# Kernel tuning notes

Measured on AMD Instinct MI355X. Metric: run time of the kernel, lower is better.

## Reference

```python
import jax, jax.numpy as jnp
import numpy as np

B, N, E = 2, 30000, 120000
IN_F, OUT_F, H = 512, 512, 4
D = OUT_F // H  # head_dim = 128
LN_EPS = 1e-5


def setup_inputs() -> dict:
    key = jax.random.key(0)
    k1, k2, k3, k4 = jax.random.split(key, 4)
    node_features = jax.random.normal(k1, (B, N, IN_F), dtype=jnp.float32)
    edge_index = jax.random.randint(k2, (2, E), 0, N, dtype=jnp.int64)
    # per-head linear transforms (bias=False): W[h] is [in_features, head_dim]
    W = jax.random.normal(k3, (H, IN_F, D), dtype=jnp.float32) / np.sqrt(IN_F)
    # per-head attention vectors a[h] is [2*head_dim] (Linear(2*head_dim,1,bias=False))
    a = jax.random.normal(k4, (H, 2 * D), dtype=jnp.float32) / np.sqrt(2 * D)
    ln_gamma = jnp.ones((OUT_F,), dtype=jnp.float32)
    ln_beta = jnp.zeros((OUT_F,), dtype=jnp.float32)
    return {"node_features": node_features, "edge_index": edge_index,
            "W": W, "a": a, "ln_gamma": ln_gamma, "ln_beta": ln_beta}


def reference(node_features, edge_index, W, a, ln_gamma, ln_beta):
    src, dst = edge_index[0], edge_index[1]
    # all-heads linear transform: [B, H, N, D]
    t = jnp.einsum('bni,hid->bhnd', node_features, W)
    # per-edge gathered features: [B, H, E, D]
    sf = t[:, :, src, :]
    df = t[:, :, dst, :]
    # attention score = [sf ; df] . a  == sf.a_src + df.a_dst  -> [B, H, E]
    scores = (jnp.einsum('bhed,hd->bhe', sf, a[:, :D])
              + jnp.einsum('bhed,hd->bhe', df, a[:, D:]))
    scores = jax.nn.leaky_relu(scores, negative_slope=0.2)
    # NOTE: faithful to source — softmax over ALL edges (dim=-1), not per-dst
    w = jax.nn.softmax(scores, axis=-1)
    # scatter-add aggregation into destination nodes (the Python-loop in torch)
    agg = jnp.zeros_like(t).at[:, :, dst, :].add(w[..., None] * sf)  # [B,H,N,D]
    # concat heads along feature dim (head order preserved)
    out = jnp.transpose(agg, (0, 2, 1, 3)).reshape(node_features.shape[0], N, H * D)
    # LayerNorm over last dim
    mu = jnp.mean(out, axis=-1, keepdims=True)
    var = jnp.mean(jnp.square(out - mu), axis=-1, keepdims=True)
    out = (out - mu) * jax.lax.rsqrt(var + LN_EPS) * ln_gamma + ln_beta
    return out
```

## Files before the change

### kernel.cpp

```cpp
#include <hip/hip_runtime.h>
#include <stdint.h>

#define Bn 2
#define Nn 30000
#define En 120000
#define KIN 512
#define Hh 4
#define Dd 128
#define MROWS 60000
#define MPAD  60032
#define LNEPS 1e-5f
#define EBLK 469

typedef unsigned short u16;
typedef unsigned int   u32;
typedef __attribute__((ext_vector_type(8))) short short8;
typedef __attribute__((ext_vector_type(4))) float f32x4;

__device__ __forceinline__ u16 f2bf(float f) {
    u32 u = __builtin_bit_cast(u32, f);
    u32 r = u + 0x7FFFu + ((u >> 16) & 1u);
    return (u16)(r >> 16);
}
__device__ __forceinline__ float bf2f(u16 h) {
    u32 u = ((u32)h) << 16;
    return __builtin_bit_cast(float, u);
}
__device__ __forceinline__ void ld16(void* lds, const void* g) {
    __builtin_amdgcn_global_load_lds((const __attribute__((address_space(1))) void*)g,
                                     (__attribute__((address_space(3))) void*)lds, 16, 0, 0);
}

__global__ void cvt_x(const float* __restrict__ x, u16* __restrict__ xb) {
    long i8 = (long)blockIdx.x * 256 + threadIdx.x;
    long base = i8 * 8;
    if (base >= (long)MPAD * KIN) return;
    short8 o = {};
    if (base < (long)MROWS * KIN) {
        const float4* px = (const float4*)(x + base);
        float4 v0 = px[0], v1 = px[1];
        o[0] = (short)f2bf(v0.x); o[1] = (short)f2bf(v0.y);
        o[2] = (short)f2bf(v0.z); o[3] = (short)f2bf(v0.w);
        o[4] = (short)f2bf(v1.x); o[5] = (short)f2bf(v1.y);
        o[6] = (short)f2bf(v1.z); o[7] = (short)f2bf(v1.w);
    }
    *(short8*)(xb + base) = o;
}

__global__ void cvt_w(const float* __restrict__ W, u16* __restrict__ wbt) {
    int idx = blockIdx.x * 256 + threadIdx.x;
    if (idx >= 512 * 512) return;
    int c = idx >> 9, i = idx & 511;
    int h = c >> 7, d = c & 127;
    wbt[idx] = f2bf(W[h * (KIN * Dd) + i * Dd + d]);
}

__launch_bounds__(256)
__global__ void gemm(const u16* __restrict__ xb, const u16* __restrict__ wbt,
                     u16* __restrict__ t) {
    __shared__ __align__(16) u16 As[128 * 32];
    __shared__ __align__(16) u16 Bs[128 * 32];
    const int tid = threadIdx.x;
    const int m0 = blockIdx.y * 128, n0 = blockIdx.x * 128;
    const int w = tid >> 6, l = tid & 63;
    const int wr = (w >> 1) * 64, wc = (w & 1) * 64;
    const int lr = l & 15, lk = l >> 4;
    f32x4 acc[4][4] = {};

    for (int k0 = 0; k0 < KIN; k0 += 32) {
        #pragma unroll
        for (int inst = 0; inst < 2; inst++) {
            int q = inst * 256 + tid;
            const u16* ga = xb  + (long)(m0 + (q >> 2)) * KIN + k0 + (q & 3) * 8;
            const u16* gb = wbt + (long)(n0 + (q >> 2)) * KIN + k0 + (q & 3) * 8;
            ld16(&As[q * 8], ga);
            ld16(&Bs[q * 8], gb);
        }
        __syncthreads();
        short8 af[4], bfr[4];
        #pragma unroll
        for (int mi = 0; mi < 4; mi++)
            af[mi] = *(const short8*)&As[(wr + mi * 16 + lr) * 32 + lk * 8];
        #pragma unroll
        for (int nj = 0; nj < 4; nj++)
            bfr[nj] = *(const short8*)&Bs[(wc + nj * 16 + lr) * 32 + lk * 8];
        #pragma unroll
        for (int mi = 0; mi < 4; mi++)
            #pragma unroll
            for (int nj = 0; nj < 4; nj++)
                acc[mi][nj] = __builtin_amdgcn_mfma_f32_16x16x32_bf16(
                    af[mi], bfr[nj], acc[mi][nj], 0, 0, 0);
        __syncthreads();
    }
    #pragma unroll
    for (int mi = 0; mi < 4; mi++)
        #pragma unroll
        for (int r = 0; r < 4; r++) {
            int row = m0 + wr + mi * 16 + lk * 4 + r;
            u16* tp = t + (long)row * 512 + n0 + wc + lr;
            #pragma unroll
            for (int nj = 0; nj < 4; nj++)
                tp[nj * 16] = f2bf(acc[mi][nj][r]);
        }
}

__global__ void s1s2_kernel(const u16* __restrict__ t, const float* __restrict__ a,
                            float* __restrict__ s1, float* __restrict__ s2) {
    int row = blockIdx.x * 4 + (threadIdx.x >> 6);
    if (row >= MROWS) return;
    int l = threadIdx.x & 63;
    int h = l >> 4, dl = (l & 15) * 8;
    short8 tv = *(const short8*)(t + (long)row * 512 + h * 128 + dl);
    const float* a1 = a + h * 256 + dl;
    const float* a2 = a1 + 128;
    float p1 = 0.f, p2 = 0.f;
    #pragma unroll
    for (int j = 0; j < 8; j++) {
        float tf = bf2f((u16)tv[j]);
        p1 += tf * a1[j];
        p2 += tf * a2[j];
    }
    #pragma unroll
    for (int off = 1; off < 16; off <<= 1) {
        p1 += __shfl_xor(p1, off, 64);
        p2 += __shfl_xor(p2, off, 64);
    }
    if ((l & 15) == 0) {
        s1[(long)row * 4 + h] = p1;
        s2[(long)row * 4 + h] = p2;
    }
}

__global__ void nodemax_kernel(const float* __restrict__ s1, const float* __restrict__ s2,
                               float* __restrict__ pmax) {
    int b = blockIdx.y, tid = threadIdx.x;
    float m1[4] = {-1e30f, -1e30f, -1e30f, -1e30f};
    float m2[4] = {-1e30f, -1e30f, -1e30f, -1e30f};
    for (int n = blockIdx.x * 256 + tid; n < Nn; n += 32 * 256) {
        float4 v1 = *(const float4*)(s1 + ((long)b * Nn + n) * 4);
        float4 v2 = *(const float4*)(s2 + ((long)b * Nn + n) * 4);
        m1[0] = fmaxf(m1[0], v1.x); m1[1] = fmaxf(m1[1], v1.y);
        m1[2] = fmaxf(m1[2], v1.z); m1[3] = fmaxf(m1[3], v1.w);
        m2[0] = fmaxf(m2[0], v2.x); m2[1] = fmaxf(m2[1], v2.y);
        m2[2] = fmaxf(m2[2], v2.z); m2[3] = fmaxf(m2[3], v2.w);
    }
    #pragma unroll
    for (int off = 1; off < 64; off <<= 1)
        #pragma unroll
        for (int h = 0; h < 4; h++) {
            m1[h] = fmaxf(m1[h], __shfl_xor(m1[h], off, 64));
            m2[h] = fmaxf(m2[h], __shfl_xor(m2[h], off, 64));
        }
    __shared__ float red[4][8];
    if ((tid & 63) == 0)
        #pragma unroll
        for (int h = 0; h < 4; h++) {
            red[tid >> 6][h] = m1[h];
            red[tid >> 6][h + 4] = m2[h];
        }
    __syncthreads();
    if (tid < 8) {
        float m = fmaxf(fmaxf(red[0][tid], red[1][tid]), fmaxf(red[2][tid], red[3][tid]));
        pmax[((b * 32 + blockIdx.x) * 8) + tid] = m;
    }
}

__global__ void mreduce_kernel(const float* __restrict__ pmax, float* __restrict__ M) {
    int tid = threadIdx.x;
    if (tid < 8) {
        int b = tid >> 2, h = tid & 3;
        float m1 = -1e30f, m2 = -1e30f;
        for (int blk = 0; blk < 32; blk++) {
            m1 = fmaxf(m1, pmax[(b * 32 + blk) * 8 + h]);
            m2 = fmaxf(m2, pmax[(b * 32 + blk) * 8 + 4 + h]);
        }
        float s = m1 + m2;
        M[tid] = s > 0.f ? s : 0.2f * s;
    }
}

__global__ void edge_kernel(const int* __restrict__ ei, const float* __restrict__ s1,
                            const float* __restrict__ s2, const float* __restrict__ M,
                            float* __restrict__ p, float* __restrict__ Zpart) {
    int e = blockIdx.x * 256 + threadIdx.x;
    int b = blockIdx.y;
    float v[4] = {0.f, 0.f, 0.f, 0.f};
    float m0 = M[b * 4 + 0], m1 = M[b * 4 + 1], m2 = M[b * 4 + 2], m3 = M[b * 4 + 3];
    if (e < En) {
        int src = ei[e], dst = ei[En + e];
        float4 v1 = *(const float4*)(s1 + ((long)b * Nn + src) * 4);
        float4 v2 = *(const float4*)(s2 + ((long)b * Nn + dst) * 4);
        float s;
        s = v1.x + v2.x; s = s > 0.f ? s : 0.2f * s; v[0] = __expf(s - m0);
        s = v1.y + v2.y; s = s > 0.f ? s : 0.2f * s; v[1] = __expf(s - m1);
        s = v1.z + v2.z; s = s > 0.f ? s : 0.2f * s; v[2] = __expf(s - m2);
        s = v1.w + v2.w; s = s > 0.f ? s : 0.2f * s; v[3] = __expf(s - m3);
        float4 o = make_float4(v[0], v[1], v[2], v[3]);
        *(float4*)(p + ((long)b * En + e) * 4) = o;
    }
    #pragma unroll
    for (int off = 1; off < 64; off <<= 1)
        #pragma unroll
        for (int h = 0; h < 4; h++)
            v[h] += __shfl_xor(v[h], off, 64);
    __shared__ float red[4][4];
    int tid = threadIdx.x;
    if ((tid & 63) == 0)
        #pragma unroll
        for (int h = 0; h < 4; h++)
            red[tid >> 6][h] = v[h];
    __syncthreads();
    if (tid < 4) {
        float z = red[0][tid] + red[1][tid] + red[2][tid] + red[3][tid];
        Zpart[((long)b * EBLK + blockIdx.x) * 4 + tid] = z;
    }
}

__global__ void zreduce_kernel(const float* __restrict__ Zpart, float* __restrict__ invZ) {
    int tid = threadIdx.x;
    int g = tid >> 6, l = tid & 63;
    int b = g >> 2, h = g & 3;
    float s = 0.f;
    for (int i = l; i < EBLK; i += 64)
        s += Zpart[((long)b * EBLK + i) * 4 + h];
    #pragma unroll
    for (int off = 1; off < 64; off <<= 1)
        s += __shfl_xor(s, off, 64);
    if (l == 0) invZ[g] = 1.0f / s;
}

__global__ void hist_kernel(const int* __restrict__ ei, int* __restrict__ deg) {
    int e = blockIdx.x * 256 + threadIdx.x;
    if (e < En) atomicAdd(&deg[ei[En + e]], 1);
}

__global__ void scan_kernel(const int* __restrict__ deg, int* __restrict__ offs,
                            int* __restrict__ cursor) {
    __shared__ int part[1024];
    int tid = threadIdx.x;
    const int CH = (Nn + 1023) / 1024;
    int start = tid * CH;
    int s = 0;
    for (int i = 0; i < CH; i++) {
        int n = start + i;
        if (n < Nn) s += deg[n];
    }
    part[tid] = s;
    __syncthreads();
    for (int off = 1; off < 1024; off <<= 1) {
        int x = (tid >= off) ? part[tid - off] : 0;
        __syncthreads();
        part[tid] += x;
        __syncthreads();
    }
    int run = part[tid] - s;
    for (int i = 0; i < CH; i++) {
        int n = start + i;
        if (n < Nn) {
            offs[n] = run;
            cursor[n] = run;
            run += deg[n];
        }
    }
    if (tid == 1023) offs[Nn] = part[1023];
}

__global__ void scatter_kernel(const int* __restrict__ ei, int* __restrict__ cursor,
                               int* __restrict__ elist) {
    int e = blockIdx.x * 256 + threadIdx.x;
    if (e < En) {
        int d = ei[En + e];
        int pos = atomicAdd(&cursor[d], 1);
        elist[pos] = e;
    }
}

__launch_bounds__(128)
__global__ void agg_kernel(const u16* __restrict__ t, const int* __restrict__ ei,
                           const float* __restrict__ p, const float* __restrict__ invZ,
                           const int* __restrict__ offs, const int* __restrict__ elist,
                           const float* __restrict__ gamma, const float* __restrict__ beta,
                           float* __restrict__ out) {
    int n = blockIdx.x, b = blockIdx.y;
    int tid = threadIdx.x;
    float invz = invZ[b * 4 + (tid >> 5)];
    int j0 = offs[n], j1 = offs[n + 1];
    const float* pb = p + (long)b * En * 4;
    const u16* tb = t + (long)b * Nn * 512;
    float a0 = 0.f, a1 = 0.f, a2 = 0.f, a3 = 0.f;
    for (int j = j0; j < j1; j++) {
        int e = elist[j];
        int src = ei[e];
        float w = pb[(long)e * 4 + (tid >> 5)] * invz;
        uint2 raw = *(const uint2*)(tb + (long)src * 512 + tid * 4);
        a0 += w * __builtin_bit_cast(float, raw.x << 16);
        a1 += w * __builtin_bit_cast(float, raw.x & 0xFFFF0000u);
        a2 += w * __builtin_bit_cast(float, raw.y << 16);
        a3 += w * __builtin_bit_cast(float, raw.y & 0xFFFF0000u);
    }
    float s  = a0 + a1 + a2 + a3;
    float ss = a0 * a0 + a1 * a1 + a2 * a2 + a3 * a3;
    #pragma unroll
    for (int off = 1; off < 64; off <<= 1) {
        s  += __shfl_xor(s, off, 64);
        ss += __shfl_xor(ss, off, 64);
    }
    __shared__ float red[4];
    if ((tid & 63) == 0) {
        red[(tid >> 6) * 2]     = s;
        red[(tid >> 6) * 2 + 1] = ss;
    }
    __syncthreads();
    s  = red[0] + red[2];
    ss = red[1] + red[3];
    float mean = s * (1.0f / 512.0f);
    float var = ss * (1.0f / 512.0f) - mean * mean;
    var = var < 0.f ? 0.f : var;
    float scale = rsqrtf(var + LNEPS);
    int c = tid * 4;
    float4 o;
    o.x = (a0 - mean) * scale * gamma[c + 0] + beta[c + 0];
    o.y = (a1 - mean) * scale * gamma[c + 1] + beta[c + 1];
    o.z = (a2 - mean) * scale * gamma[c + 2] + beta[c + 2];
    o.w = (a3 - mean) * scale * gamma[c + 3] + beta[c + 3];
    *(float4*)(out + ((long)b * Nn + n) * 512 + c) = o;
}

extern "C" void kernel_launch(void* const* d_in, const int* in_sizes, int n_in,
                              void* d_out, int out_size, void* d_ws, size_t ws_size,
                              hipStream_t stream) {
    const float* x     = (const float*)d_in[0];
    const int*   ei    = (const int*)d_in[1];
    const float* W     = (const float*)d_in[2];
    const float* a     = (const float*)d_in[3];
    const float* gamma = (const float*)d_in[4];
    const float* beta  = (const float*)d_in[5];
    float* out = (float*)d_out;

    char* ws = (char*)d_ws;
    size_t off = 0;
    auto alloc = [&](size_t bytes) -> void* {
        void* ptr = ws + off;
        off = (off + bytes + 255) & ~(size_t)255;
        return ptr;
    };
    u16*   xb     = (u16*)alloc((size_t)MPAD * KIN * 2);
    u16*   wbt    = (u16*)alloc((size_t)512 * 512 * 2);
    u16*   t      = (u16*)alloc((size_t)MPAD * 512 * 2);
    float* s1     = (float*)alloc((size_t)MROWS * 4 * 4);
    float* s2     = (float*)alloc((size_t)MROWS * 4 * 4);
    float* p      = (float*)alloc((size_t)Bn * En * 4 * 4);
    float* pmax   = (float*)alloc((size_t)Bn * 32 * 8 * 4);
    float* M      = (float*)alloc(8 * 4);
    float* Zpart  = (float*)alloc((size_t)Bn * EBLK * 4 * 4);
    float* invZ   = (float*)alloc(8 * 4);
    int*   deg    = (int*)alloc((size_t)Nn * 4);
    int*   offs   = (int*)alloc((size_t)(Nn + 1) * 4);
    int*   cursor = (int*)alloc((size_t)Nn * 4);
    int*   elist  = (int*)alloc((size_t)En * 4);

    hipMemsetAsync(deg, 0, (size_t)Nn * 4, stream);

    cvt_x<<<(int)(((long)MPAD * KIN / 8 + 255) / 256), 256, 0, stream>>>(x, xb);
    cvt_w<<<(512 * 512) / 256, 256, 0, stream>>>(W, wbt);
    gemm<<<dim3(4, MPAD / 128), 256, 0, stream>>>(xb, wbt, t);
    s1s2_kernel<<<MROWS / 4, 256, 0, stream>>>(t, a, s1, s2);
    nodemax_kernel<<<dim3(32, Bn), 256, 0, stream>>>(s1, s2, pmax);
    mreduce_kernel<<<1, 64, 0, stream>>>(pmax, M);
    edge_kernel<<<dim3(EBLK, Bn), 256, 0, stream>>>(ei, s1, s2, M, p, Zpart);
    zreduce_kernel<<<1, 512, 0, stream>>>(Zpart, invZ);
    hist_kernel<<<(En + 255) / 256, 256, 0, stream>>>(ei, deg);
    scan_kernel<<<1, 1024, 0, stream>>>(deg, offs, cursor);
    scatter_kernel<<<(En + 255) / 256, 256, 0, stream>>>(ei, cursor, elist);
    agg_kernel<<<dim3(Nn, Bn), 128, 0, stream>>>(t, ei, p, invZ, offs, elist, gamma, beta, out);
}
```

Before: 436.6 us.

## Fuse attention score dot products into GEMM epilogue and presort edge weights for aggregation

```diff
diff --git a/kernel.cpp b/kernel.cpp
--- a/kernel.cpp
+++ b/kernel.cpp
@@ -22,9 +22,11 @@
     u32 r = u + 0x7FFFu + ((u >> 16) & 1u);
     return (u16)(r >> 16);
 }
-__device__ __forceinline__ float bf2f(u16 h) {
-    u32 u = ((u32)h) << 16;
-    return __builtin_bit_cast(float, u);
+__device__ __forceinline__ float bflo(u32 u) {
+    return __builtin_bit_cast(float, u << 16);
+}
+__device__ __forceinline__ float bfhi(u32 u) {
+    return __builtin_bit_cast(float, u & 0xFFFF0000u);
 }
 __device__ __forceinline__ void ld16(void* lds, const void* g) {
     __builtin_amdgcn_global_load_lds((const __attribute__((address_space(1))) void*)g,
@@ -57,9 +59,11 @@
 
 __launch_bounds__(256)
 __global__ void gemm(const u16* __restrict__ xb, const u16* __restrict__ wbt,
-                     u16* __restrict__ t) {
+                     const float* __restrict__ ag, u16* __restrict__ t,
+                     float* __restrict__ s1g, float* __restrict__ s2g) {
     __shared__ __align__(16) u16 As[128 * 32];
     __shared__ __align__(16) u16 Bs[128 * 32];
+    __shared__ float sred[2][2][128];
     const int tid = threadIdx.x;
     const int m0 = blockIdx.y * 128, n0 = blockIdx.x * 128;
     const int w = tid >> 6, l = tid & 63;
@@ -71,10 +75,10 @@
         #pragma unroll
         for (int inst = 0; inst < 2; inst++) {
             int q = inst * 256 + tid;
-            const u16* ga = xb  + (long)(m0 + (q >> 2)) * KIN + k0 + (q & 3) * 8;
-            const u16* gb = wbt + (long)(n0 + (q >> 2)) * KIN + k0 + (q & 3) * 8;
-            ld16(&As[q * 8], ga);
-            ld16(&Bs[q * 8], gb);
+            const u16* gap = xb  + (long)(m0 + (q >> 2)) * KIN + k0 + (q & 3) * 8;
+            const u16* gbp = wbt + (long)(n0 + (q >> 2)) * KIN + k0 + (q & 3) * 8;
+            ld16(&As[q * 8], gap);
+            ld16(&Bs[q * 8], gbp);
         }
         __syncthreads();
         short8 af[4], bfr[4];
@@ -102,32 +106,52 @@
             for (int nj = 0; nj < 4; nj++)
                 tp[nj * 16] = f2bf(acc[mi][nj][r]);
         }
-}
-
-__global__ void s1s2_kernel(const u16* __restrict__ t, const float* __restrict__ a,
-                            float* __restrict__ s1, float* __restrict__ s2) {
-    int row = blockIdx.x * 4 + (threadIdx.x >> 6);
-    if (row >= MROWS) return;
-    int l = threadIdx.x & 63;
-    int h = l >> 4, dl = (l & 15) * 8;
-    short8 tv = *(const short8*)(t + (long)row * 512 + h * 128 + dl);
-    const float* a1 = a + h * 256 + dl;
-    const float* a2 = a1 + 128;
-    float p1 = 0.f, p2 = 0.f;
-    #pragma unroll
-    for (int j = 0; j < 8; j++) {
-        float tf = bf2f((u16)tv[j]);
-        p1 += tf * a1[j];
-        p2 += tf * a2[j];
-    }
-    #pragma unroll
-    for (int off = 1; off < 16; off <<= 1) {
-        p1 += __shfl_xor(p1, off, 64);
-        p2 += __shfl_xor(p2, off, 64);
-    }
-    if ((l & 15) == 0) {
-        s1[(long)row * 4 + h] = p1;
-        s2[(long)row * 4 + h] = p2;
+    const int h = n0 >> 7;
+    float a1c[4], a2c[4];
+    #pragma unroll
+    for (int nj = 0; nj < 4; nj++) {
+        int col = wc + nj * 16 + lr;
+        a1c[nj] = ag[h * 256 + col];
+        a2c[nj] = ag[h * 256 + 128 + col];
+    }
+    float p1[16], p2[16];
+    #pragma unroll
+    for (int mi = 0; mi < 4; mi++)
+        #pragma unroll
+        for (int r = 0; r < 4; r++) {
+            float v1 = 0.f, v2 = 0.f;
+            #pragma unroll
+            for (int nj = 0; nj < 4; nj++) {
+                float tv = acc[mi][nj][r];
+                v1 += tv * a1c[nj];
+                v2 += tv * a2c[nj];
+            }
+            p1[mi * 4 + r] = v1;
+            p2[mi * 4 + r] = v2;
+        }
+    #pragma unroll
+    for (int off = 1; off < 16; off <<= 1)
+        #pragma unroll
+        for (int i = 0; i < 16; i++) {
+            p1[i] += __shfl_xor(p1[i], off, 64);
+            p2[i] += __shfl_xor(p2[i], off, 64);
+        }
+    if (lr == 0)
+        #pragma unroll
+        for (int mi = 0; mi < 4; mi++)
+            #pragma unroll
+            for (int r = 0; r < 4; r++) {
+                int row = wr + mi * 16 + lk * 4 + r;
+                sred[0][w & 1][row] = p1[mi * 4 + r];
+                sred[1][w & 1][row] = p2[mi * 4 + r];
+            }
+    __syncthreads();
+    if (tid < 128) {
+        int row = m0 + tid;
+        if (row < MROWS) {
+            s1g[(long)row * 4 + h] = sred[0][0][tid] + sred[0][1][tid];
+            s2g[(long)row * 4 + h] = sred[1][0][tid] + sred[1][1][tid];
+        }
     }
 }
 
@@ -265,39 +289,60 @@
     if (tid == 1023) offs[Nn] = part[1023];
 }
 
-__global__ void scatter_kernel(const int* __restrict__ ei, int* __restrict__ cursor,
-                               int* __restrict__ elist) {
+__global__ void scatter_kernel(const int* __restrict__ ei, const float* __restrict__ p,
+                               int* __restrict__ cursor, int* __restrict__ srcs,
+                               float* __restrict__ pw) {
     int e = blockIdx.x * 256 + threadIdx.x;
-    if (e < En) {
-        int d = ei[En + e];
-        int pos = atomicAdd(&cursor[d], 1);
-        elist[pos] = e;
-    }
-}
-
-__launch_bounds__(128)
-__global__ void agg_kernel(const u16* __restrict__ t, const int* __restrict__ ei,
-                           const float* __restrict__ p, const float* __restrict__ invZ,
-                           const int* __restrict__ offs, const int* __restrict__ elist,
+    if (e >= En) return;
+    int src = ei[e], dst = ei[En + e];
+    int pos = atomicAdd(&cursor[dst], 1);
+    srcs[pos] = src;
+    *(float4*)(pw + (long)pos * 4)        = *(const float4*)(p + (long)e * 4);
+    *(float4*)(pw + ((long)En + pos) * 4) = *(const float4*)(p + ((long)En + e) * 4);
+}
+
+__launch_bounds__(256)
+__global__ void agg_kernel(const u16* __restrict__ t, const int* __restrict__ srcs,
+                           const float* __restrict__ pw, const float* __restrict__ invZ,
+                           const int* __restrict__ offs,
                            const float* __restrict__ gamma, const float* __restrict__ beta,
                            float* __restrict__ out) {
-    int n = blockIdx.x, b = blockIdx.y;
     int tid = threadIdx.x;
-    float invz = invZ[b * 4 + (tid >> 5)];
+    int lid = tid & 127;
+    int n = blockIdx.x * 2 + (tid >> 7);
+    int b = blockIdx.y;
+    int h = lid >> 5;
     int j0 = offs[n], j1 = offs[n + 1];
-    const float* pb = p + (long)b * En * 4;
+    const float* pwb = pw + (long)b * En * 4;
     const u16* tb = t + (long)b * Nn * 512;
     float a0 = 0.f, a1 = 0.f, a2 = 0.f, a3 = 0.f;
-    for (int j = j0; j < j1; j++) {
-        int e = elist[j];
-        int src = ei[e];
-        float w = pb[(long)e * 4 + (tid >> 5)] * invz;
-        uint2 raw = *(const uint2*)(tb + (long)src * 512 + tid * 4);
-        a0 += w * __builtin_bit_cast(float, raw.x << 16);
-        a1 += w * __builtin_bit_cast(float, raw.x & 0xFFFF0000u);
-        a2 += w * __builtin_bit_cast(float, raw.y << 16);
-        a3 += w * __builtin_bit_cast(float, raw.y & 0xFFFF0000u);
-    }
+    int j = j0;
+    for (; j + 4 <= j1; j += 4) {
+        int s0 = srcs[j], s1i = srcs[j + 1], s2i = srcs[j + 2], s3i = srcs[j + 3];
+        float w0 = pwb[(long)j * 4 + h];
+        float w1 = pwb[(long)(j + 1) * 4 + h];
+        float w2 = pwb[(long)(j + 2) * 4 + h];
+        float w3 = pwb[(long)(j + 3) * 4 + h];
+        uint2 r0 = *(const uint2*)(tb + (long)s0 * 512 + lid * 4);
+        uint2 r1 = *(const uint2*)(tb + (long)s1i * 512 + lid * 4);
+        uint2 r2 = *(const uint2*)(tb + (long)s2i * 512 + lid * 4);
+        uint2 r3 = *(const uint2*)(tb + (long)s3i * 512 + lid * 4);
+        a0 += w0 * bflo(r0.x) + w1 * bflo(r1.x) + w2 * bflo(r2.x) + w3 * bflo(r3.x);
+        a1 += w0 * bfhi(r0.x) + w1 * bfhi(r1.x) + w2 * bfhi(r2.x) + w3 * bfhi(r3.x);
+        a2 += w0 * bflo(r0.y) + w1 * bflo(r1.y) + w2 * bflo(r2.y) + w3 * bflo(r3.y);
+        a3 += w0 * bfhi(r0.y) + w1 * bfhi(r1.y) + w2 * bfhi(r2.y) + w3 * bfhi(r3.y);
+    }
+    for (; j < j1; j++) {
+        int s0 = srcs[j];
+        float w0 = pwb[(long)j * 4 + h];
+        uint2 r0 = *(const uint2*)(tb + (long)s0 * 512 + lid * 4);
+        a0 += w0 * bflo(r0.x);
+        a1 += w0 * bfhi(r0.x);
+        a2 += w0 * bflo(r0.y);
+        a3 += w0 * bfhi(r0.y);
+    }
+    float invz = invZ[b * 4 + h];
+    a0 *= invz; a1 *= invz; a2 *= invz; a3 *= invz;
     float s  = a0 + a1 + a2 + a3;
     float ss = a0 * a0 + a1 * a1 + a2 * a2 + a3 * a3;
     #pragma unroll
@@ -305,19 +350,18 @@
         s  += __shfl_xor(s, off, 64);
         ss += __shfl_xor(ss, off, 64);
     }
-    __shared__ float red[4];
-    if ((tid & 63) == 0) {
-        red[(tid >> 6) * 2]     = s;
-        red[(tid >> 6) * 2 + 1] = ss;
-    }
+    __shared__ float red[4][2];
+    int wv = tid >> 6;
+    if ((tid & 63) == 0) { red[wv][0] = s; red[wv][1] = ss; }
     __syncthreads();
-    s  = red[0] + red[2];
-    ss = red[1] + red[3];
+    int base = (tid >> 7) * 2;
+    s  = red[base][0] + red[base + 1][0];
+    ss = red[base][1] + red[base + 1][1];
     float mean = s * (1.0f / 512.0f);
     float var = ss * (1.0f / 512.0f) - mean * mean;
     var = var < 0.f ? 0.f : var;
     float scale = rsqrtf(var + LNEPS);
-    int c = tid * 4;
+    int c = lid * 4;
     float4 o;
     o.x = (a0 - mean) * scale * gamma[c + 0] + beta[c + 0];
     o.y = (a1 - mean) * scale * gamma[c + 1] + beta[c + 1];
@@ -350,6 +394,7 @@
     float* s1     = (float*)alloc((size_t)MROWS * 4 * 4);
     float* s2     = (float*)alloc((size_t)MROWS * 4 * 4);
     float* p      = (float*)alloc((size_t)Bn * En * 4 * 4);
+    float* pw     = (float*)alloc((size_t)Bn * En * 4 * 4);
     float* pmax   = (float*)alloc((size_t)Bn * 32 * 8 * 4);
     float* M      = (float*)alloc(8 * 4);
     float* Zpart  = (float*)alloc((size_t)Bn * EBLK * 4 * 4);
@@ -357,20 +402,19 @@
     int*   deg    = (int*)alloc((size_t)Nn * 4);
     int*   offs   = (int*)alloc((size_t)(Nn + 1) * 4);
     int*   cursor = (int*)alloc((size_t)Nn * 4);
-    int*   elist  = (int*)alloc((size_t)En * 4);
+    int*   srcs   = (int*)alloc((size_t)En * 4);
 
     hipMemsetAsync(deg, 0, (size_t)Nn * 4, stream);
 
     cvt_x<<<(int)(((long)MPAD * KIN / 8 + 255) / 256), 256, 0, stream>>>(x, xb);
     cvt_w<<<(512 * 512) / 256, 256, 0, stream>>>(W, wbt);
-    gemm<<<dim3(4, MPAD / 128), 256, 0, stream>>>(xb, wbt, t);
-    s1s2_kernel<<<MROWS / 4, 256, 0, stream>>>(t, a, s1, s2);
+    gemm<<<dim3(4, MPAD / 128), 256, 0, stream>>>(xb, wbt, a, t, s1, s2);
     nodemax_kernel<<<dim3(32, Bn), 256, 0, stream>>>(s1, s2, pmax);
     mreduce_kernel<<<1, 64, 0, stream>>>(pmax, M);
     edge_kernel<<<dim3(EBLK, Bn), 256, 0, stream>>>(ei, s1, s2, M, p, Zpart);
     zreduce_kernel<<<1, 512, 0, stream>>>(Zpart, invZ);
     hist_kernel<<<(En + 255) / 256, 256, 0, stream>>>(ei, deg);
     scan_kernel<<<1, 1024, 0, stream>>>(deg, offs, cursor);
-    scatter_kernel<<<(En + 255) / 256, 256, 0, stream>>>(ei, cursor, elist);
-    agg_kernel<<<dim3(Nn, Bn), 128, 0, stream>>>(t, ei, p, invZ, offs, elist, gamma, beta, out);
-}
+    scatter_kernel<<<(En + 255) / 256, 256, 0, stream>>>(ei, p, cursor, srcs, pw);
+    agg_kernel<<<dim3(Nn / 2, Bn), 256, 0, stream>>>(t, srcs, pw, invZ, offs, gamma, beta, out);
+}
```

Measured after the change: 429.4 us. No clear change (-1.6%).
